# Kernel optimization log

Measured on AMD Instinct MI355X. Metric: run time of the kernel, lower is better.

Reference implementation:

```python
import jax, jax.numpy as jnp
import numpy as np

LN_EPS = 1e-5

def _layernorm(x, w, b):
    mu = jnp.mean(x, axis=-1, keepdims=True)
    var = jnp.mean((x - mu) ** 2, axis=-1, keepdims=True)
    return (x - mu) * jax.lax.rsqrt(var + LN_EPS) * w + b

def _parallel_scan(A, B, x):
    # A, B, x: (Bb, L, S). Log-space cumsum trick, faithful to torch version.
    A_safe = jnp.clip(A, 0.001, 0.999)
    log_A = jnp.log(A_safe + 1e-10)
    log_cum_A = jnp.cumsum(log_A, axis=1)
    log_cum_A_max = jnp.max(log_cum_A, axis=1, keepdims=True)
    log_cum_A_c = log_cum_A - log_cum_A_max
    cum_A = jnp.exp(log_cum_A_c)
    BX = B * x
    # shifted (exclusive) centered log-cumsum: zeros at t=0
    zeros = jnp.zeros_like(log_cum_A_c[:, :1])
    log_cum_shift = jnp.concatenate([zeros, log_cum_A_c[:, :-1]], axis=1)
    BX_norm = BX * jnp.exp(-log_cum_shift)
    cum_BX = jnp.cumsum(BX_norm, axis=1)
    return cum_BX * cum_A

def setup_inputs() -> dict:
    key = jax.random.key(0)
    ks = jax.random.split(key, 8)
    Bb, L, D, S = 16, 4096, 512, 64
    def xavier(k, shape, gain):
        fan_out, fan_in = shape
        std = gain * np.sqrt(2.0 / (fan_in + fan_out))
        return jax.random.normal(k, shape, jnp.float32) * std
    x = jax.random.normal(ks[0], (Bb, L, D), jnp.float32)
    Wx = xavier(ks[1], (S, D), 0.5)
    Wdt = xavier(ks[2], (S, D), 1.0)
    WB = xavier(ks[3], (S, D), 0.4)
    WC = xavier(ks[4], (S, D), 0.4)
    Wout = xavier(ks[5], (D, S), 0.5)
    # A_init = -rand*0.8 - 0.2 ; A_log = log(-A_init) = log(uniform(0.2, 1.0))
    A_log = jnp.log(jax.random.uniform(ks[6], (S,), jnp.float32, 0.2, 1.0))
    return {
        "x": x,
        "ln_w": jnp.ones((D,), jnp.float32),
        "ln_b": jnp.zeros((D,), jnp.float32),
        "Wx": Wx, "bx": jnp.zeros((S,), jnp.float32),
        "Wdt": Wdt, "bdt": jnp.zeros((S,), jnp.float32),
        "A_log": A_log,
        "WB": WB, "WC": WC,
        "Dp": jnp.zeros((D,), jnp.float32),
        "Wout": Wout, "bout": jnp.zeros((D,), jnp.float32),
    }

def reference(x, ln_w, ln_b, Wx, bx, Wdt, bdt, A_log, WB, WC, Dp, Wout, bout):
    x_norm = _layernorm(x, ln_w, ln_b)                       # (B,L,D)
    delta = jax.nn.softplus(x_norm @ Wdt.T + bdt) * 0.01 + 0.0001  # (B,L,S)
    B_t = x_norm @ WB.T                                      # (B,L,S)
    C_t = x_norm @ WC.T                                      # (B,L,S)
    A = -jnp.exp(A_log)                                      # (S,)
    x_proj = x_norm @ Wx.T + bx                              # (B,L,S)
    deltaA = jnp.clip(delta * A, -10.0, -0.0001)
    A_disc = jnp.exp(deltaA)
    B_disc = delta * B_t
    h = _parallel_scan(A_disc, B_disc, x_proj)               # (B,L,S)
    y = C_t * h
    y = jnp.where(jnp.any(~jnp.isfinite(y)), jnp.zeros_like(y), y)
    y = y @ Wout.T + bout                                    # (B,L,D)
    D_safe = jnp.clip(Dp, -2.0, 2.0)
    return y + D_safe * x
```

## Files before the change

kernel.cpp:

```cpp
#include <hip/hip_runtime.h>
#include <math.h>

typedef __attribute__((ext_vector_type(4))) float  floatx4;
typedef __attribute__((ext_vector_type(8))) short  shortx8;
typedef unsigned short ushort_t;
typedef unsigned int   uint32;

#define BB 16
#define LL 4096
#define DD 512
#define SS 64
#define NTOK (BB*LL)
#define NCH 64

__device__ __forceinline__ ushort_t f2bf(float f) {
    uint32 u = __float_as_uint(f);
    u += 0x7FFFu + ((u >> 16) & 1u);
    return (ushort_t)(u >> 16);
}
__device__ __forceinline__ float bf2f(ushort_t u) {
    return __uint_as_float(((uint32)u) << 16);
}

__device__ __forceinline__ void gload16(const void* g, void* l) {
    __builtin_amdgcn_global_load_lds(
        (const __attribute__((address_space(1))) unsigned int*)g,
        (__attribute__((address_space(3))) unsigned int*)l, 16, 0, 0);
}

__global__ __launch_bounds__(256) void k_prep(
    const float* __restrict__ Wdt, const float* __restrict__ WB,
    const float* __restrict__ WC,  const float* __restrict__ Wx,
    const float* __restrict__ Wout,
    ushort_t* __restrict__ wcat, ushort_t* __restrict__ woutb)
{
    int tid = blockIdx.x * 256 + threadIdx.x;
    int n = tid >> 9, k = tid & 511;
    const float* src = (n < 64) ? Wdt : (n < 128) ? WB : (n < 192) ? WC : Wx;
    wcat[tid] = f2bf(src[(n & 63) * 512 + k]);
    if (tid < 512 * 64) woutb[tid] = f2bf(Wout[tid]);
}

__global__ __launch_bounds__(256) void k_ln(
    const float* __restrict__ x, const float* __restrict__ lnw, const float* __restrict__ lnb,
    ushort_t* __restrict__ xn)
{
    const int wave = threadIdx.x >> 6, lane = threadIdx.x & 63;
    const int tok = blockIdx.x * 4 + wave;
    const float4* xr = (const float4*)(x + (size_t)tok * DD);
    float4 a = xr[lane * 2], b = xr[lane * 2 + 1];
    float s = a.x + a.y + a.z + a.w + b.x + b.y + b.z + b.w;
    float q = a.x*a.x + a.y*a.y + a.z*a.z + a.w*a.w
            + b.x*b.x + b.y*b.y + b.z*b.z + b.w*b.w;
    #pragma unroll
    for (int off = 32; off > 0; off >>= 1) {
        s += __shfl_xor(s, off);
        q += __shfl_xor(q, off);
    }
    float mu = s * (1.0f / 512.0f);
    float rs = rsqrtf(q * (1.0f / 512.0f) - mu * mu + 1e-5f);
    float4 wa = ((const float4*)lnw)[lane * 2], wb = ((const float4*)lnw)[lane * 2 + 1];
    float4 ba = ((const float4*)lnb)[lane * 2], bb = ((const float4*)lnb)[lane * 2 + 1];
    uint4 pk;
    pk.x = (uint32)f2bf((a.x - mu) * rs * wa.x + ba.x) | ((uint32)f2bf((a.y - mu) * rs * wa.y + ba.y) << 16);
    pk.y = (uint32)f2bf((a.z - mu) * rs * wa.z + ba.z) | ((uint32)f2bf((a.w - mu) * rs * wa.w + ba.w) << 16);
    pk.z = (uint32)f2bf((b.x - mu) * rs * wb.x + bb.x) | ((uint32)f2bf((b.y - mu) * rs * wb.y + bb.y) << 16);
    pk.w = (uint32)f2bf((b.z - mu) * rs * wb.z + bb.z) | ((uint32)f2bf((b.w - mu) * rs * wb.w + bb.w) << 16);
    ((uint4*)(xn + (size_t)tok * DD))[lane] = pk;
}

__global__ __launch_bounds__(512, 4) void k_proj(
    const ushort_t* __restrict__ xn, const ushort_t* __restrict__ wcat,
    const float* __restrict__ bdt, const float* __restrict__ bx_, const float* __restrict__ A_log,
    float* __restrict__ Ap, float* __restrict__ BXv, ushort_t* __restrict__ Ctb,
    float* __restrict__ Asum, float* __restrict__ Bsum)
{
    __shared__ __align__(16) char sBuf[49152];
    ushort_t* sA = (ushort_t*)sBuf;
    ushort_t* sB = (ushort_t*)(sBuf + 16384);
    float*    sPA = (float*)sBuf;
    float*    sPB = sPA + 2 * 64 * 17;

    const int tid  = threadIdx.x;
    const int wave = tid >> 6, lane = tid & 63;
    const int ln   = lane & 15, qd = lane >> 4;
    const int mh   = wave >> 2, nq = wave & 3;
    const int token0 = blockIdx.x * 128;

    int tA[2], cA[2], tB[4], cB[4];
    #pragma unroll
    for (int r = 0; r < 2; r++) { int sl = r * 512 + tid; tA[r] = sl >> 3; cA[r] = ((sl & 7) ^ (tA[r] & 7)) * 8; }
    #pragma unroll
    for (int r = 0; r < 4; r++) { int sl = r * 512 + tid; tB[r] = sl >> 3; cB[r] = ((sl & 7) ^ (tB[r] & 7)) * 8; }

    floatx4 acc[4][4] = {};

    for (int kc = 0; kc < 8; kc++) {
        const int kb = kc * 64;
        #pragma unroll
        for (int r = 0; r < 2; r++)
            gload16(xn + (size_t)(token0 + tA[r]) * DD + kb + cA[r],
                    sBuf + r * 8192 + wave * 1024);
        #pragma unroll
        for (int r = 0; r < 4; r++)
            gload16(wcat + (size_t)tB[r] * DD + kb + cB[r],
                    sBuf + 16384 + r * 8192 + wave * 1024);
        __syncthreads();
        #pragma unroll
        for (int ks8 = 0; ks8 < 8; ks8 += 4) {
            shortx8 af[4], bf[4];
            #pragma unroll
            for (int mt = 0; mt < 4; mt++) {
                int t = mh * 64 + mt * 16 + ln;
                af[mt] = *(const shortx8*)&sA[t * 64 + (((ks8 + qd) ^ (ln & 7)) << 3)];
            }
            #pragma unroll
            for (int nt = 0; nt < 4; nt++) {
                int n = nt * 64 + nq * 16 + ln;
                bf[nt] = *(const shortx8*)&sB[n * 64 + (((ks8 + qd) ^ (ln & 7)) << 3)];
            }
            #pragma unroll
            for (int mt = 0; mt < 4; mt++)
                #pragma unroll
                for (int nt = 0; nt < 4; nt++)
                    acc[mt][nt] = __builtin_amdgcn_mfma_f32_16x16x32_bf16(
                        af[mt], bf[nt], acc[mt][nt], 0, 0, 0);
        }
        __syncthreads();
    }

    {
        const int s = nq * 16 + ln;
        float bdt_s = bdt[s], bx_s = bx_[s];
        float A_s = -expf(A_log[s]);
        const bool fc = ((blockIdx.x & 31) == 0) && (mh == 0);
        #pragma unroll
        for (int mt = 0; mt < 4; mt++) {
            float Al = 1.f, Bl = 0.f;
            #pragma unroll
            for (int r = 0; r < 4; r++) {
                int tl  = mt * 16 + qd * 4 + r;
                int tok = token0 + mh * 64 + tl;
                float zdt = acc[mt][0][r];
                float zb  = acc[mt][1][r];
                float zc  = acc[mt][2][r];
                float zx  = acc[mt][3][r];
                float zin = zdt + bdt_s;
                float sp  = fmaxf(zin, 0.0f) + log1pf(expf(-fabsf(zin)));
                float delta = sp * 0.01f + 1e-4f;
                float dA    = fminf(fmaxf(delta * A_s, -10.0f), -1e-4f);
                float a     = fminf(fmaxf(expf(dA), 0.001f), 0.999f) + 1e-10f;
                float bxv   = delta * zb * (zx + bx_s);
                size_t g = (size_t)tok * 64 + s;
                Ap[g] = a; BXv[g] = bxv; Ctb[g] = f2bf(zc);
                bool first = fc && (tl == 0);
                float alpha = first ? 0.f : a;
                float beta  = first ? bxv : a * bxv;
                Al *= alpha;
                Bl = fmaf(alpha, Bl, beta);
            }
            sPA[(mh * 64 + s) * 17 + mt * 4 + qd] = Al;
            sPB[(mh * 64 + s) * 17 + mt * 4 + qd] = Bl;
        }
    }
    __syncthreads();
    if (tid < 128) {
        int ch = tid >> 6, ss = tid & 63;
        const float* pa = &sPA[(ch * 64 + ss) * 17];
        const float* pb = &sPB[(ch * 64 + ss) * 17];
        float A = pa[0], B = pb[0];
        #pragma unroll
        for (int g = 1; g < 16; g++) {
            A *= pa[g];
            B = fmaf(pa[g], B, pb[g]);
        }
        int o = (blockIdx.x * 2 + ch) * 64 + ss;
        Asum[o] = A; Bsum[o] = B;
    }
}

__global__ __launch_bounds__(256) void k_scan(
    const float* __restrict__ Ap, const float* __restrict__ BXv, const ushort_t* __restrict__ Ctb,
    const float* __restrict__ Asum, const float* __restrict__ Bsum,
    ushort_t* __restrict__ P)
{
    __shared__ float sAs[4096], sBs[4096];
    const int tid = threadIdx.x;
    const int b = blockIdx.x >> 4, cq = blockIdx.x & 15;
    #pragma unroll
    for (int i = 0; i < 16; i++) {
        int idx = i * 256 + tid;
        sAs[idx] = Asum[b * 4096 + idx];
        sBs[idx] = Bsum[b * 4096 + idx];
    }
    __syncthreads();
    const int w = tid >> 6, s = tid & 63;
    const int c = cq * 4 + w;
    float h = 0.f;
    for (int cc = 0; cc < c; cc++)
        h = fmaf(sAs[cc * 64 + s], h, sBs[cc * 64 + s]);
    size_t base = ((size_t)b * LL + c * 64) * 64 + s;
    const bool fc = (c == 0);
    #pragma unroll 8
    for (int t = 0; t < 64; t++) {
        float a = Ap[base + (size_t)t * 64];
        float v = BXv[base + (size_t)t * 64];
        float alpha = (fc && t == 0) ? 0.f : a;
        float beta  = (fc && t == 0) ? v   : a * v;
        h = fmaf(alpha, h, beta);
        P[base + (size_t)t * 64] = f2bf(bf2f(Ctb[base + (size_t)t * 64]) * h);
    }
}

__global__ __launch_bounds__(256, 4) void k_gemm2(
    const ushort_t* __restrict__ P, const ushort_t* __restrict__ woutb,
    const float* __restrict__ bout, const float* __restrict__ Dp,
    const float* __restrict__ x, float* __restrict__ out)
{
    __shared__ __align__(16) char sPBuf[8192];
    __shared__ __align__(16) float sOut[16 * 260];
    ushort_t* sP = (ushort_t*)sPBuf;

    const int tid  = threadIdx.x;
    const int wave = tid >> 6, lane = tid & 63;
    const int ln   = lane & 15, qd = lane >> 4;
    const int nq   = wave;
    const int token0 = blockIdx.x * 64;

    #pragma unroll
    for (int r = 0; r < 2; r++) {
        int sl = r * 256 + tid;
        int t = sl >> 3, k8 = (sl & 7) ^ (t & 7);
        gload16(P + (size_t)(token0 + t) * 64 + k8 * 8,
                sPBuf + r * 4096 + wave * 1024);
    }
    __syncthreads();

    #pragma unroll
    for (int half = 0; half < 2; half++) {
        const int nh = half * 256;
        floatx4 acc[4][4] = {};
        #pragma unroll
        for (int ks8 = 0; ks8 < 8; ks8 += 4) {
            shortx8 af[4], bf[4];
            #pragma unroll
            for (int mt = 0; mt < 4; mt++) {
                int t = mt * 16 + ln;
                af[mt] = *(const shortx8*)&sP[t * 64 + (((ks8 + qd) ^ (ln & 7)) << 3)];
            }
            #pragma unroll
            for (int nt = 0; nt < 4; nt++) {
                int d = nh + nq * 64 + nt * 16 + ln;
                bf[nt] = *(const shortx8*)(woutb + (size_t)d * 64 + (ks8 + qd) * 8);
            }
            #pragma unroll
            for (int mt = 0; mt < 4; mt++)
                #pragma unroll
                for (int nt = 0; nt < 4; nt++)
                    acc[mt][nt] = __builtin_amdgcn_mfma_f32_16x16x32_bf16(
                        af[mt], bf[nt], acc[mt][nt], 0, 0, 0);
        }

        for (int mt = 0; mt < 4; mt++) {
            __syncthreads();
            #pragma unroll
            for (int nt = 0; nt < 4; nt++)
                #pragma unroll
                for (int r = 0; r < 4; r++)
                    sOut[(qd * 4 + r) * 260 + nq * 64 + nt * 16 + ln] = acc[mt][nt][r];
            __syncthreads();
            #pragma unroll
            for (int i = 0; i < 4; i++) {
                int idx = i * 256 + tid;
                int row = idx >> 6, c4 = (idx & 63) * 4;
                int tok = token0 + mt * 16 + row;
                int d   = nh + c4;
                float4 o  = *(float4*)&sOut[row * 260 + c4];
                float4 xv = *(const float4*)(x + (size_t)tok * DD + d);
                float4 bo = *(const float4*)(bout + d);
                float4 dp = *(const float4*)(Dp + d);
                float4 res;
                res.x = fmaf(fminf(fmaxf(dp.x, -2.f), 2.f), xv.x, o.x + bo.x);
                res.y = fmaf(fminf(fmaxf(dp.y, -2.f), 2.f), xv.y, o.y + bo.y);
                res.z = fmaf(fminf(fmaxf(dp.z, -2.f), 2.f), xv.z, o.z + bo.z);
                res.w = fmaf(fminf(fmaxf(dp.w, -2.f), 2.f), xv.w, o.w + bo.w);
                *(float4*)(out + (size_t)tok * DD + d) = res;
            }
        }
    }
}

extern "C" void kernel_launch(void* const* d_in, const int* in_sizes, int n_in,
                              void* d_out, int out_size, void* d_ws, size_t ws_size,
                              hipStream_t stream)
{
    const float* x     = (const float*)d_in[0];
    const float* lnw   = (const float*)d_in[1];
    const float* lnb   = (const float*)d_in[2];
    const float* Wx    = (const float*)d_in[3];
    const float* bx_   = (const float*)d_in[4];
    const float* Wdt   = (const float*)d_in[5];
    const float* bdt   = (const float*)d_in[6];
    const float* A_log = (const float*)d_in[7];
    const float* WB    = (const float*)d_in[8];
    const float* WC    = (const float*)d_in[9];
    const float* Dp    = (const float*)d_in[10];
    const float* Wout  = (const float*)d_in[11];
    const float* bout  = (const float*)d_in[12];
    float* out = (float*)d_out;

    char* w = (char*)d_ws;
    constexpr size_t SZ_XN = (size_t)NTOK * DD * 2;
    constexpr size_t SZ_T  = (size_t)NTOK * 64 * 4;
    ushort_t* xn    = (ushort_t*)(w);
    ushort_t* Pm    = (ushort_t*)(w);
    float*    Ap    = (float*)(w + SZ_XN);
    float*    BXv   = (float*)(w + SZ_XN + SZ_T);
    ushort_t* Ctb   = (ushort_t*)(w + SZ_XN + 2 * SZ_T);
    float*    Asum  = (float*)(w + SZ_XN + 3 * SZ_T);
    float*    Bsum  = (float*)(w + SZ_XN + 3 * SZ_T + 262144);
    ushort_t* Wcat  = (ushort_t*)(w + SZ_XN + 3 * SZ_T + 2 * 262144);
    ushort_t* WoutB = (ushort_t*)(w + SZ_XN + 3 * SZ_T + 2 * 262144 + 262144);

    k_prep<<<512, 256, 0, stream>>>(Wdt, WB, WC, Wx, Wout, Wcat, WoutB);
    k_ln<<<NTOK / 4, 256, 0, stream>>>(x, lnw, lnb, xn);
    k_proj<<<NTOK / 128, 512, 0, stream>>>(xn, Wcat, bdt, bx_, A_log,
                                           Ap, BXv, Ctb, Asum, Bsum);
    k_scan<<<BB * 16, 256, 0, stream>>>(Ap, BXv, Ctb, Asum, Bsum, Pm);
    k_gemm2<<<NTOK / 64, 256, 0, stream>>>(Pm, WoutB, bout, Dp, x, out);
}
```

Measured before the change: 361.3 us.

## Fuse layernorm into projection GEMM by folding LN weights and correcting afterwards

Removes the separate layernorm kernel and the bf16 normalized activation buffer. The projection kernel now reads raw fp32 x, converts it to bf16 into shared memory while accumulating per-token sum and sum-of-squares, and applies mean/rstd afterwards as a rank-1 correction using precomputed per-column weight sums (u) and bias dot-products (c). LN weight is folded into the bf16 projection weights in the prep kernel, which is also vectorized. This saves a full write and read of the normalized tensor, at the cost of extra fp32 global traffic inside the GEMM loop and bf16 rounding applied to un-centered x, which can reduce accuracy.

```diff
diff --git a/kernel.cpp b/kernel.cpp
--- a/kernel.cpp
+++ b/kernel.cpp
@@ -1,4 +1,5 @@
 #include <hip/hip_runtime.h>
+#include <hip/hip_bf16.h>
 #include <math.h>
 
 typedef __attribute__((ext_vector_type(4))) float  floatx4;
@@ -21,6 +22,11 @@
 __device__ __forceinline__ float bf2f(ushort_t u) {
     return __uint_as_float(((uint32)u) << 16);
 }
+__device__ __forceinline__ uint32 pack2(float lo, float hi) {
+    __hip_bfloat162 h = __float22bfloat162_rn(make_float2(lo, hi));
+    union { __hip_bfloat162 h; uint32 u; } cv; cv.h = h;
+    return cv.u;
+}
 
 __device__ __forceinline__ void gload16(const void* g, void* l) {
     __builtin_amdgcn_global_load_lds(
@@ -32,50 +38,61 @@
     const float* __restrict__ Wdt, const float* __restrict__ WB,
     const float* __restrict__ WC,  const float* __restrict__ Wx,
     const float* __restrict__ Wout,
-    ushort_t* __restrict__ wcat, ushort_t* __restrict__ woutb)
-{
-    int tid = blockIdx.x * 256 + threadIdx.x;
-    int n = tid >> 9, k = tid & 511;
-    const float* src = (n < 64) ? Wdt : (n < 128) ? WB : (n < 192) ? WC : Wx;
-    wcat[tid] = f2bf(src[(n & 63) * 512 + k]);
-    if (tid < 512 * 64) woutb[tid] = f2bf(Wout[tid]);
-}
-
-__global__ __launch_bounds__(256) void k_ln(
-    const float* __restrict__ x, const float* __restrict__ lnw, const float* __restrict__ lnb,
-    ushort_t* __restrict__ xn)
-{
-    const int wave = threadIdx.x >> 6, lane = threadIdx.x & 63;
-    const int tok = blockIdx.x * 4 + wave;
-    const float4* xr = (const float4*)(x + (size_t)tok * DD);
-    float4 a = xr[lane * 2], b = xr[lane * 2 + 1];
-    float s = a.x + a.y + a.z + a.w + b.x + b.y + b.z + b.w;
-    float q = a.x*a.x + a.y*a.y + a.z*a.z + a.w*a.w
-            + b.x*b.x + b.y*b.y + b.z*b.z + b.w*b.w;
-    #pragma unroll
-    for (int off = 32; off > 0; off >>= 1) {
-        s += __shfl_xor(s, off);
-        q += __shfl_xor(q, off);
-    }
-    float mu = s * (1.0f / 512.0f);
-    float rs = rsqrtf(q * (1.0f / 512.0f) - mu * mu + 1e-5f);
-    float4 wa = ((const float4*)lnw)[lane * 2], wb = ((const float4*)lnw)[lane * 2 + 1];
-    float4 ba = ((const float4*)lnb)[lane * 2], bb = ((const float4*)lnb)[lane * 2 + 1];
-    uint4 pk;
-    pk.x = (uint32)f2bf((a.x - mu) * rs * wa.x + ba.x) | ((uint32)f2bf((a.y - mu) * rs * wa.y + ba.y) << 16);
-    pk.y = (uint32)f2bf((a.z - mu) * rs * wa.z + ba.z) | ((uint32)f2bf((a.w - mu) * rs * wa.w + ba.w) << 16);
-    pk.z = (uint32)f2bf((b.x - mu) * rs * wb.x + bb.x) | ((uint32)f2bf((b.y - mu) * rs * wb.y + bb.y) << 16);
-    pk.w = (uint32)f2bf((b.z - mu) * rs * wb.z + bb.z) | ((uint32)f2bf((b.w - mu) * rs * wb.w + bb.w) << 16);
-    ((uint4*)(xn + (size_t)tok * DD))[lane] = pk;
+    const float* __restrict__ lnw, const float* __restrict__ lnb,
+    ushort_t* __restrict__ wcat, ushort_t* __restrict__ woutb,
+    float* __restrict__ u, float* __restrict__ c)
+{
+    const int bid = blockIdx.x;
+    if (bid < 64) {
+        const int wave = threadIdx.x >> 6, lane = threadIdx.x & 63;
+        const int n = bid * 4 + wave;
+        const float* src = (n < 64) ? Wdt : (n < 128) ? WB : (n < 192) ? WC : Wx;
+        const float* row = src + (size_t)(n & 63) * 512;
+        float4 a  = *(const float4*)(row + lane * 8);
+        float4 b  = *(const float4*)(row + lane * 8 + 4);
+        float4 wa = *(const float4*)(lnw + lane * 8);
+        float4 wb = *(const float4*)(lnw + lane * 8 + 4);
+        float4 ba = *(const float4*)(lnb + lane * 8);
+        float4 bb = *(const float4*)(lnb + lane * 8 + 4);
+        float w0 = a.x * wa.x, w1 = a.y * wa.y, w2 = a.z * wa.z, w3 = a.w * wa.w;
+        float w4 = b.x * wb.x, w5 = b.y * wb.y, w6 = b.z * wb.z, w7 = b.w * wb.w;
+        float us = w0 + w1 + w2 + w3 + w4 + w5 + w6 + w7;
+        float cs = a.x*ba.x + a.y*ba.y + a.z*ba.z + a.w*ba.w
+                 + b.x*bb.x + b.y*bb.y + b.z*bb.z + b.w*bb.w;
+        uint4 o;
+        o.x = (uint32)f2bf(w0) | ((uint32)f2bf(w1) << 16);
+        o.y = (uint32)f2bf(w2) | ((uint32)f2bf(w3) << 16);
+        o.z = (uint32)f2bf(w4) | ((uint32)f2bf(w5) << 16);
+        o.w = (uint32)f2bf(w6) | ((uint32)f2bf(w7) << 16);
+        ((uint4*)(wcat + (size_t)n * 512))[lane] = o;
+        #pragma unroll
+        for (int off = 32; off > 0; off >>= 1) {
+            us += __shfl_xor(us, off);
+            cs += __shfl_xor(cs, off);
+        }
+        if (lane == 0) { u[n] = us; c[n] = cs; }
+    } else {
+        int idx = (bid - 64) * 2048 + threadIdx.x * 8;
+        float4 a = *(const float4*)(Wout + idx);
+        float4 b = *(const float4*)(Wout + idx + 4);
+        uint4 o;
+        o.x = (uint32)f2bf(a.x) | ((uint32)f2bf(a.y) << 16);
+        o.y = (uint32)f2bf(a.z) | ((uint32)f2bf(a.w) << 16);
+        o.z = (uint32)f2bf(b.x) | ((uint32)f2bf(b.y) << 16);
+        o.w = (uint32)f2bf(b.z) | ((uint32)f2bf(b.w) << 16);
+        *(uint4*)(woutb + idx) = o;
+    }
 }
 
 __global__ __launch_bounds__(512, 4) void k_proj(
-    const ushort_t* __restrict__ xn, const ushort_t* __restrict__ wcat,
+    const float* __restrict__ x, const ushort_t* __restrict__ wcat,
+    const float* __restrict__ u, const float* __restrict__ c,
     const float* __restrict__ bdt, const float* __restrict__ bx_, const float* __restrict__ A_log,
     float* __restrict__ Ap, float* __restrict__ BXv, ushort_t* __restrict__ Ctb,
     float* __restrict__ Asum, float* __restrict__ Bsum)
 {
     __shared__ __align__(16) char sBuf[49152];
+    __shared__ float sMu[128], sRs[128];
     ushort_t* sA = (ushort_t*)sBuf;
     ushort_t* sB = (ushort_t*)(sBuf + 16384);
     float*    sPA = (float*)sBuf;
@@ -87,24 +104,36 @@
     const int mh   = wave >> 2, nq = wave & 3;
     const int token0 = blockIdx.x * 128;
 
-    int tA[2], cA[2], tB[4], cB[4];
-    #pragma unroll
-    for (int r = 0; r < 2; r++) { int sl = r * 512 + tid; tA[r] = sl >> 3; cA[r] = ((sl & 7) ^ (tA[r] & 7)) * 8; }
+    int tB[4], cB[4];
     #pragma unroll
     for (int r = 0; r < 4; r++) { int sl = r * 512 + tid; tB[r] = sl >> 3; cB[r] = ((sl & 7) ^ (tB[r] & 7)) * 8; }
+    int rowA[2], k8A[2];
+    #pragma unroll
+    for (int r = 0; r < 2; r++) { int sl = r * 512 + tid; rowA[r] = sl >> 3; k8A[r] = sl & 7; }
 
     floatx4 acc[4][4] = {};
+    float sacc[2] = {0.f, 0.f}, qacc[2] = {0.f, 0.f};
 
     for (int kc = 0; kc < 8; kc++) {
         const int kb = kc * 64;
-        #pragma unroll
-        for (int r = 0; r < 2; r++)
-            gload16(xn + (size_t)(token0 + tA[r]) * DD + kb + cA[r],
-                    sBuf + r * 8192 + wave * 1024);
         #pragma unroll
         for (int r = 0; r < 4; r++)
             gload16(wcat + (size_t)tB[r] * DD + kb + cB[r],
                     sBuf + 16384 + r * 8192 + wave * 1024);
+        #pragma unroll
+        for (int r = 0; r < 2; r++) {
+            const float4* xp = (const float4*)(x + (size_t)(token0 + rowA[r]) * DD + kb + k8A[r] * 8);
+            float4 v0 = xp[0], v1 = xp[1];
+            sacc[r] += (v0.x + v0.y) + (v0.z + v0.w) + (v1.x + v1.y) + (v1.z + v1.w);
+            qacc[r] += v0.x*v0.x + v0.y*v0.y + v0.z*v0.z + v0.w*v0.w
+                     + v1.x*v1.x + v1.y*v1.y + v1.z*v1.z + v1.w*v1.w;
+            uint4 pk;
+            pk.x = pack2(v0.x, v0.y);
+            pk.y = pack2(v0.z, v0.w);
+            pk.z = pack2(v1.x, v1.y);
+            pk.w = pack2(v1.z, v1.w);
+            *(uint4*)(sBuf + rowA[r] * 128 + ((k8A[r] ^ (rowA[r] & 7)) << 4)) = pk;
+        }
         __syncthreads();
         #pragma unroll
         for (int ks8 = 0; ks8 < 8; ks8 += 4) {
@@ -129,10 +158,27 @@
         __syncthreads();
     }
 
+    #pragma unroll
+    for (int r = 0; r < 2; r++) {
+        float s_ = sacc[r], q_ = qacc[r];
+        s_ += __shfl_xor(s_, 1); q_ += __shfl_xor(q_, 1);
+        s_ += __shfl_xor(s_, 2); q_ += __shfl_xor(q_, 2);
+        s_ += __shfl_xor(s_, 4); q_ += __shfl_xor(q_, 4);
+        if ((lane & 7) == 0) {
+            int row = r * 64 + wave * 8 + (lane >> 3);
+            float mu = s_ * (1.0f / 512.0f);
+            sMu[row] = mu;
+            sRs[row] = rsqrtf(q_ * (1.0f / 512.0f) - mu * mu + 1e-5f);
+        }
+    }
+    __syncthreads();
+
     {
         const int s = nq * 16 + ln;
         float bdt_s = bdt[s], bx_s = bx_[s];
         float A_s = -expf(A_log[s]);
+        float u0 = u[s], u1 = u[64 + s], u2 = u[128 + s], u3 = u[192 + s];
+        float c0 = c[s], c1 = c[64 + s], c2 = c[128 + s], c3 = c[192 + s];
         const bool fc = ((blockIdx.x & 31) == 0) && (mh == 0);
         #pragma unroll
         for (int mt = 0; mt < 4; mt++) {
@@ -141,10 +187,11 @@
             for (int r = 0; r < 4; r++) {
                 int tl  = mt * 16 + qd * 4 + r;
                 int tok = token0 + mh * 64 + tl;
-                float zdt = acc[mt][0][r];
-                float zb  = acc[mt][1][r];
-                float zc  = acc[mt][2][r];
-                float zx  = acc[mt][3][r];
+                float mu_t = sMu[mh * 64 + tl], rs_t = sRs[mh * 64 + tl];
+                float zdt = rs_t * (acc[mt][0][r] - mu_t * u0) + c0;
+                float zb  = rs_t * (acc[mt][1][r] - mu_t * u1) + c1;
+                float zc  = rs_t * (acc[mt][2][r] - mu_t * u2) + c2;
+                float zx  = rs_t * (acc[mt][3][r] - mu_t * u3) + c3;
                 float zin = zdt + bdt_s;
                 float sp  = fmaxf(zin, 0.0f) + log1pf(expf(-fabsf(zin)));
                 float delta = sp * 0.01f + 1e-4f;
@@ -312,7 +359,6 @@
     char* w = (char*)d_ws;
     constexpr size_t SZ_XN = (size_t)NTOK * DD * 2;
     constexpr size_t SZ_T  = (size_t)NTOK * 64 * 4;
-    ushort_t* xn    = (ushort_t*)(w);
     ushort_t* Pm    = (ushort_t*)(w);
     float*    Ap    = (float*)(w + SZ_XN);
     float*    BXv   = (float*)(w + SZ_XN + SZ_T);
@@ -321,10 +367,11 @@
     float*    Bsum  = (float*)(w + SZ_XN + 3 * SZ_T + 262144);
     ushort_t* Wcat  = (ushort_t*)(w + SZ_XN + 3 * SZ_T + 2 * 262144);
     ushort_t* WoutB = (ushort_t*)(w + SZ_XN + 3 * SZ_T + 2 * 262144 + 262144);
-
-    k_prep<<<512, 256, 0, stream>>>(Wdt, WB, WC, Wx, Wout, Wcat, WoutB);
-    k_ln<<<NTOK / 4, 256, 0, stream>>>(x, lnw, lnb, xn);
-    k_proj<<<NTOK / 128, 512, 0, stream>>>(xn, Wcat, bdt, bx_, A_log,
+    float*    Uc    = (float*)(w + SZ_XN + 3 * SZ_T + 2 * 262144 + 262144 + 65536);
+    float*    Cc    = Uc + 256;
+
+    k_prep<<<80, 256, 0, stream>>>(Wdt, WB, WC, Wx, Wout, lnw, lnb, Wcat, WoutB, Uc, Cc);
+    k_proj<<<NTOK / 128, 512, 0, stream>>>(x, Wcat, Uc, Cc, bdt, bx_, A_log,
                                            Ap, BXv, Ctb, Asum, Bsum);
     k_scan<<<BB * 16, 256, 0, stream>>>(Ap, BXv, Ctb, Asum, Bsum, Pm);
     k_gemm2<<<NTOK / 64, 256, 0, stream>>>(Pm, WoutB, bout, Dp, x, out);
```

After: 343.4 us. -5.0%, faster.
